# Kernel optimization log

Measured on AMD Instinct MI355X. Metric: run time of the kernel, lower is better.

The kernel has to match this reference:

```python
import jax, jax.numpy as jnp
import numpy as np

B, S, D, H = 2, 2048, 1024, 16
DK = D // H
DFF = 4 * D
EPS = 1e-6


def layer_norm(x, gamma, beta):
    mu = jnp.mean(x, axis=-1, keepdims=True)
    var = jnp.mean(jnp.square(x - mu), axis=-1, keepdims=True)
    return (x - mu) * jax.lax.rsqrt(var + EPS) * gamma + beta


def setup_inputs() -> dict:
    key = jax.random.key(0)
    ks = jax.random.split(key, 10)
    xavier = (6.0 / (D + D)) ** 0.5
    kaiming = (6.0 / D) ** 0.5
    kaiming2 = (6.0 / DFF) ** 0.5
    return {
        "batch_X": jax.random.normal(ks[0], (B, S, D), dtype=jnp.float32),
        "padding_mask": jax.random.randint(ks[1], (B, S), 0, 2, dtype=jnp.int32),
        "W_Q": jax.random.uniform(ks[2], (D, D), jnp.float32, -xavier, xavier),
        "W_K": jax.random.uniform(ks[3], (D, D), jnp.float32, -xavier, xavier),
        "W_V": jax.random.uniform(ks[4], (D, D), jnp.float32, -xavier, xavier),
        "W_O": jax.random.uniform(ks[5], (D, D), jnp.float32, -xavier, xavier),
        "W1": jax.random.uniform(ks[6], (D, DFF), jnp.float32, -kaiming, kaiming),
        "b1": jnp.zeros((DFF,), jnp.float32),
        "W2": jax.random.uniform(ks[7], (DFF, D), jnp.float32, -kaiming2, kaiming2),
        "b2": jnp.zeros((D,), jnp.float32),
        "gamma1": jnp.ones((D,), jnp.float32),
        "beta1": jnp.zeros((D,), jnp.float32),
        "gamma2": jnp.ones((D,), jnp.float32),
        "beta2": jnp.zeros((D,), jnp.float32),
    }


def reference(batch_X, padding_mask, W_Q, W_K, W_V, W_O, W1, b1, W2, b2,
              gamma1, beta1, gamma2, beta2):
    x = batch_X
    b, s, d = x.shape

    # --- multi-head self-attention (use_mask=False: padding mask only) ---
    q = (x @ W_Q).reshape(b, s, H, DK)
    k = (x @ W_K).reshape(b, s, H, DK)
    v = (x @ W_V).reshape(b, s, H, DK)
    scores = jnp.einsum("bqhd,bkhd->bhqk", q, k) / jnp.sqrt(jnp.float32(DK))
    # mask[b,i,j] = (padding_mask[b,i] == 0) for all j: whole query rows are
    # either fully masked (softmax -> NaN -> zeroed in the original) or
    # fully unmasked. Equivalent math: softmax then zero padded query rows.
    probs = jax.nn.softmax(scores, axis=-1)
    keep = (padding_mask != 0).astype(probs.dtype)[:, None, :, None]  # [B,1,S,1]
    probs = probs * keep
    ctx = jnp.einsum("bhqk,bkhd->bqhd", probs, v).reshape(b, s, d)
    attn_out = ctx @ W_O

    # --- residual + LN (dropout identity in eval) ---
    x = x + layer_norm(attn_out, gamma1, beta1)

    # --- FFN ---
    h = jax.nn.relu(x @ W1 + b1)
    ffn_out = h @ W2 + b2
    x = x + layer_norm(ffn_out, gamma2, beta2)
    return x
```

## Files before the change

kernel.cpp:

```cpp
#include <hip/hip_runtime.h>
#include <hip/hip_bf16.h>

#define B 2
#define S 2048
#define D 1024
#define H 16
#define DKh 64
#define DFF 4096
#define M (B*S)

typedef unsigned short u16;
typedef unsigned int u32;
typedef __attribute__((ext_vector_type(8))) short short8;
typedef __attribute__((ext_vector_type(4))) float f32x4;

__device__ __forceinline__ u16 f2bf(float f) {
  union { float f; unsigned u; } v; v.f = f;
  unsigned r = v.u + 0x7fffu + ((v.u >> 16) & 1u);
  return (u16)(r >> 16);
}

__device__ __forceinline__ float bf2f(u16 h) {
  union { u32 u; float f; } v; v.u = ((u32)h) << 16; return v.f;
}

__device__ __forceinline__ u32 pkbf2(float a, float b) {
  __hip_bfloat162 h = __float22bfloat162_rn(make_float2(a, b));
  return *reinterpret_cast<u32*>(&h);
}

__device__ __forceinline__ void gload16(const void* g, void* l) {
  __builtin_amdgcn_global_load_lds((const __attribute__((address_space(1))) void*)g,
                                   (__attribute__((address_space(3))) void*)l, 16, 0, 0);
}

#define SBAR()  __builtin_amdgcn_sched_barrier(0)
#define WBAR()  __builtin_amdgcn_s_barrier()

__device__ __forceinline__ void tcvt_body(const float* __restrict__ W,
    u16* __restrict__ Wt, int K, int N, int n0, int k0, u16 (*l)[65]) {
  const int tx = threadIdx.x & 63, ty = threadIdx.x >> 6;
#pragma unroll
  for (int j = 0; j < 16; ++j) {
    int r = j * 4 + ty;
    l[r][tx] = f2bf(W[(size_t)(k0 + r) * N + n0 + tx]);
  }
  __syncthreads();
#pragma unroll
  for (int j = 0; j < 16; ++j) {
    int r = j * 4 + ty;
    Wt[(size_t)(n0 + r) * K + k0 + tx] = l[tx][r];
  }
}

__global__ __launch_bounds__(256) void prep(const float* __restrict__ X,
    u16* __restrict__ Xb, const float* __restrict__ Wq, const float* __restrict__ Wk,
    const float* __restrict__ Wv, const float* __restrict__ Wo,
    u16* __restrict__ dQKV, u16* __restrict__ dO,
    const float* __restrict__ W1, u16* __restrict__ W1t,
    const float* __restrict__ W2, u16* __restrict__ W2t) {
  __shared__ u16 l[64][65];
  const int bid = blockIdx.x;
  if (bid < 4096) {
    int i = bid * 256 + threadIdx.x;
    float4 v = ((const float4*)X)[i];
    ushort4 o = make_ushort4(f2bf(v.x), f2bf(v.y), f2bf(v.z), f2bf(v.w));
    ((ushort4*)Xb)[i] = o;
  } else if (bid < 5120) {
    int bid2 = bid - 4096;
    int z = bid2 >> 8, r2 = bid2 & 255;
    const float* W = (z == 0) ? Wq : (z == 1) ? Wk : (z == 2) ? Wv : Wo;
    u16* Wt = (z < 3) ? dQKV + (size_t)z * D * D : dO;
    tcvt_body(W, Wt, D, D, (r2 & 15) * 64, (r2 >> 4) * 64, l);
  } else if (bid < 6144) {
    int r2 = bid - 5120;
    tcvt_body(W1, W1t, D, DFF, (r2 & 63) * 64, (r2 >> 6) * 64, l);
  } else {
    int r2 = bid - 6144;
    tcvt_body(W2, W2t, DFF, D, (r2 & 15) * 64, (r2 >> 4) * 64, l);
  }
}

__global__ __launch_bounds__(256) void vtrans(const u16* __restrict__ V,
                                              u16* __restrict__ Vt, int ld) {
  __shared__ u16 l[64][65];
  const int s0 = blockIdx.x * 64, by = blockIdx.y;
  const int b = by >> 4, h = by & 15;
  const int tx = threadIdx.x & 63, ty = threadIdx.x >> 6;
#pragma unroll
  for (int j = 0; j < 16; ++j) {
    int r = j * 4 + ty;
    l[r][tx] = V[(size_t)(b * S + s0 + r) * ld + h * DKh + tx];
  }
  __syncthreads();
#pragma unroll
  for (int j = 0; j < 16; ++j) {
    int r = j * 4 + ty;
    Vt[(size_t)(by * 64 + r) * S + s0 + tx] = l[tx][r];
  }
}

template<int EPI>
__global__ __launch_bounds__(512, 2) void gemm256(const u16* __restrict__ Ag,
    const u16* __restrict__ Bg, void* __restrict__ Cout,
    const float* __restrict__ bias, int Mm, int N, int ld, int Kper,
    int sCols, float qscl) {
  __shared__ u16 lA[2 * 16384];
  __shared__ u16 lB[2 * 16384];
  const int t = threadIdx.x;
  const int lane = t & 63, w = t >> 6;
  const int wm = w >> 2, wn = w & 3;
  const int g = lane >> 4, c = lane & 15;
  const int swz = (c & 7) << 4;

  const int gx = gridDim.x, gy = gridDim.y;
  const int orig = blockIdx.y * gx + blockIdx.x;
  const int qchunk = (gx * gy) >> 3;
  const int wg = (orig & 7) * qchunk + (orig >> 3);
  const int bn0 = (wg % gx) * 256, bm0 = (wg / gx) * 256;
  const int koff = blockIdx.z * Kper;
  const int nk = Kper >> 6;

  f32x4 acc[8][4] = {};
  short8 af[4][2], bf[2][2];

  auto stageA = [&](int h, int buf, int kt) {
#pragma unroll
    for (int i = 0; i < 2; ++i) {
      int chunk = i * 512 + t;
      int rh = chunk >> 3;
      int cb = (chunk & 7) * 16;
      int r = (rh & 63) + (h + 2 * (rh >> 6)) * 64;
      gload16(Ag + (size_t)(bm0 + r) * ld + koff + kt * 64 + ((cb ^ ((r & 7) << 4)) >> 1),
              (void*)((char*)lA + buf * 32768 + h * 16384 + chunk * 16));
    }
  };
  auto stageB = [&](int h, int buf, int kt) {
#pragma unroll
    for (int i = 0; i < 2; ++i) {
      int chunk = i * 512 + t;
      int rh = chunk >> 3;
      int cb = (chunk & 7) * 16;
      int r = (rh & 31) + (h + 2 * (rh >> 5)) * 32;
      gload16(Bg + (size_t)(bn0 + r) * ld + koff + kt * 64 + ((cb ^ ((r & 7) << 4)) >> 1),
              (void*)((char*)lB + buf * 32768 + h * 16384 + chunk * 16));
    }
  };

#define RDA(mh) { const char* lab = (const char*)lA + cur * 32768;                          \
  _Pragma("unroll") for (int mt2 = 0; mt2 < 4; ++mt2)                                       \
    _Pragma("unroll") for (int kc = 0; kc < 2; ++kc)                                        \
      af[mt2][kc] = *(const short8*)(lab + (wm * 64 + (mh) * 128 + mt2 * 16 + c) * 128      \
                                         + ((kc * 64 + g * 16) ^ swz)); }
#define RDB(nh) { const char* lbb = (const char*)lB + cur * 32768;                          \
  _Pragma("unroll") for (int nt2 = 0; nt2 < 2; ++nt2)                                       \
    _Pragma("unroll") for (int kc = 0; kc < 2; ++kc)                                        \
      bf[nt2][kc] = *(const short8*)(lbb + ((nh) * 128 + wn * 32 + nt2 * 16 + c) * 128      \
                                         + ((kc * 64 + g * 16) ^ swz)); }
#define QMFMA(mh, nh) { __builtin_amdgcn_s_setprio(1);                                      \
  _Pragma("unroll") for (int mt2 = 0; mt2 < 4; ++mt2)                                       \
    _Pragma("unroll") for (int nt2 = 0; nt2 < 2; ++nt2)                                     \
      _Pragma("unroll") for (int kc = 0; kc < 2; ++kc)                                      \
        acc[(mh) * 4 + mt2][(nh) * 2 + nt2] = __builtin_amdgcn_mfma_f32_16x16x32_bf16(      \
            af[mt2][kc], bf[nt2][kc], acc[(mh) * 4 + mt2][(nh) * 2 + nt2], 0, 0, 0);        \
  __builtin_amdgcn_s_setprio(0); }

  stageA(0, 0, 0); stageB(0, 0, 0); stageA(1, 0, 0); stageB(1, 0, 0);
  asm volatile("s_waitcnt vmcnt(4)" ::: "memory");
  SBAR(); WBAR(); SBAR();

  int cur = 0;
  for (int kt = 0; kt < nk; ++kt) {
    const bool more = (kt + 1 < nk);
    RDB(0); RDA(0);
    if (more) { stageA(0, cur ^ 1, kt + 1);
                asm volatile("s_waitcnt vmcnt(4)" ::: "memory"); }
    else      { asm volatile("s_waitcnt vmcnt(2)" ::: "memory"); }
    SBAR(); WBAR(); SBAR();
    QMFMA(0, 0);
    SBAR(); WBAR(); SBAR();
    RDA(1);
    if (more) { stageB(0, cur ^ 1, kt + 1);
                asm volatile("s_waitcnt vmcnt(4)" ::: "memory"); }
    else      { asm volatile("s_waitcnt vmcnt(0)" ::: "memory"); }
    SBAR(); WBAR(); SBAR();
    QMFMA(1, 0);
    SBAR(); WBAR(); SBAR();
    RDB(1);
    if (more) stageA(1, cur ^ 1, kt + 1);
    SBAR(); WBAR(); SBAR();
    QMFMA(1, 1);
    SBAR(); WBAR(); SBAR();
    RDA(0);
    if (more) { stageB(1, cur ^ 1, kt + 1);
                asm volatile("s_waitcnt vmcnt(4)" ::: "memory"); }
    SBAR(); WBAR(); SBAR();
    QMFMA(0, 1);
    SBAR(); WBAR(); SBAR();
    cur ^= 1;
  }
#undef RDA
#undef RDB
#undef QMFMA

  float* plane = (EPI == 1) ? ((float*)Cout + (size_t)blockIdx.z * Mm * N) : (float*)Cout;
#pragma unroll
  for (int mt = 0; mt < 8; ++mt) {
#pragma unroll
    for (int nt = 0; nt < 4; ++nt) {
      const int col = bn0 + wn * 64 + nt * 16 + c;
      float bv = (EPI == 2) ? bias[col] : 0.0f;
#pragma unroll
      for (int r = 0; r < 4; ++r) {
        const int row = bm0 + wm * 128 + mt * 16 + g * 4 + r;
        float v = acc[mt][nt][r];
        if (EPI == 2) v = fmaxf(v + bv, 0.0f);
        if (EPI == 0 && col < sCols) v *= qscl;
        if (EPI == 1) plane[(size_t)row * N + col] = v;
        else          ((u16*)Cout)[(size_t)row * N + col] = f2bf(v);
      }
    }
  }
}

__global__ __launch_bounds__(256) void attn_kernel(const u16* __restrict__ Q,
    const u16* __restrict__ Kp, const u16* __restrict__ Vt,
    const int* __restrict__ mask, u16* __restrict__ Ctx, int ldq) {
  __shared__ u16 lK[2][64 * 64];
  __shared__ u16 lV[2][64 * 64];
  __shared__ u16 lP[4 * 16 * 64];
  const int t = threadIdx.x, lane = t & 63, w = t >> 6;
  const int g = lane >> 4, c = lane & 15;
  const int gx = gridDim.x;
  const int orig = blockIdx.y * gx + blockIdx.x;
  const int qchunk = (gx * gridDim.y) >> 3;
  const int wg = (orig & 7) * qchunk + (orig >> 3);
  const int bx = wg % gx, by = wg / gx;
  const int b = by >> 4, h = by & 15;
  const int q0w = bx * 128 + w * 16;

  short8 qf[2][2];
#pragma unroll
  for (int s = 0; s < 2; ++s)
#pragma unroll
    for (int kc = 0; kc < 2; ++kc)
      qf[s][kc] = *(const short8*)&Q[(size_t)(b * S + q0w + s * 64 + c) * ldq + h * DKh + kc * 32 + g * 8];

  float lsum0 = 0.0f, lsum1 = 0.0f;
  f32x4 accO0[4] = {}, accO1[4] = {};

  auto stage = [&](int buf, int it) {
    const int kv0 = it * 64;
#pragma unroll
    for (int q = 0; q < 2; ++q) {
      int idx = q * 256 + t;
      int row = idx >> 3;
      int colb = (idx & 7) * 16;
      int scol = colb ^ ((row & 7) << 4);
      gload16(Kp + (size_t)(b * S + kv0 + row) * ldq + h * DKh + scol / 2,
              (void*)(&lK[buf][0] + idx * 8));
      gload16(Vt + (size_t)(by * 64 + row) * S + kv0 + scol / 2,
              (void*)(&lV[buf][0] + idx * 8));
    }
  };

  stage(0, 0);
  int cur = 0;
  for (int it = 0; it < S / 64; ++it) {
    __syncthreads();
    if (it + 1 < S / 64) stage(cur ^ 1, it + 1);

    f32x4 sc0[4], sc1[4];
#pragma unroll
    for (int ct = 0; ct < 4; ++ct) {
      int row = ct * 16 + c;
      short8 kf0 = *(const short8*)&lK[cur][row * 64 + (((0 * 64 + g * 16) ^ ((row & 7) << 4)) >> 1)];
      short8 kf1 = *(const short8*)&lK[cur][row * 64 + (((1 * 64 + g * 16) ^ ((row & 7) << 4)) >> 1)];
      f32x4 z0 = {0.f, 0.f, 0.f, 0.f};
      z0 = __builtin_amdgcn_mfma_f32_16x16x32_bf16(kf0, qf[0][0], z0, 0, 0, 0);
      z0 = __builtin_amdgcn_mfma_f32_16x16x32_bf16(kf1, qf[0][1], z0, 0, 0, 0);
      sc0[ct] = z0;
      f32x4 z1 = {0.f, 0.f, 0.f, 0.f};
      z1 = __builtin_amdgcn_mfma_f32_16x16x32_bf16(kf0, qf[1][0], z1, 0, 0, 0);
      z1 = __builtin_amdgcn_mfma_f32_16x16x32_bf16(kf1, qf[1][1], z1, 0, 0, 0);
      sc1[ct] = z1;
    }

    short8 pa0[2], pa1[2];
#pragma unroll
    for (int ct = 0; ct < 4; ++ct) {
      float p0 = __builtin_amdgcn_exp2f(sc0[ct][0]);
      float p1 = __builtin_amdgcn_exp2f(sc0[ct][1]);
      float p2 = __builtin_amdgcn_exp2f(sc0[ct][2]);
      float p3 = __builtin_amdgcn_exp2f(sc0[ct][3]);
      lsum0 += (p0 + p1) + (p2 + p3);
      uint2 pk;
      pk.x = pkbf2(p0, p1);
      pk.y = pkbf2(p2, p3);
      *(uint2*)&lP[w * 1024 + c * 64 + (((ct * 32 + g * 8) ^ ((c & 7) << 4)) >> 1)] = pk;
    }
#pragma unroll
    for (int kc = 0; kc < 2; ++kc)
      pa0[kc] = *(const short8*)&lP[w * 1024 + c * 64 + (((kc * 64 + g * 16) ^ ((c & 7) << 4)) >> 1)];
#pragma unroll
    for (int ct = 0; ct < 4; ++ct) {
      float p0 = __builtin_amdgcn_exp2f(sc1[ct][0]);
      float p1 = __builtin_amdgcn_exp2f(sc1[ct][1]);
      float p2 = __builtin_amdgcn_exp2f(sc1[ct][2]);
      float p3 = __builtin_amdgcn_exp2f(sc1[ct][3]);
      lsum1 += (p0 + p1) + (p2 + p3);
      uint2 pk;
      pk.x = pkbf2(p0, p1);
      pk.y = pkbf2(p2, p3);
      *(uint2*)&lP[w * 1024 + c * 64 + (((ct * 32 + g * 8) ^ ((c & 7) << 4)) >> 1)] = pk;
    }
#pragma unroll
    for (int kc = 0; kc < 2; ++kc)
      pa1[kc] = *(const short8*)&lP[w * 1024 + c * 64 + (((kc * 64 + g * 16) ^ ((c & 7) << 4)) >> 1)];

#pragma unroll
    for (int dt = 0; dt < 4; ++dt) {
#pragma unroll
      for (int kc = 0; kc < 2; ++kc) {
        int rowV = dt * 16 + c;
        int bcolV = (kc * 64 + g * 16) ^ ((rowV & 7) << 4);
        short8 vb = *(const short8*)&lV[cur][rowV * 64 + bcolV / 2];
        accO0[dt] = __builtin_amdgcn_mfma_f32_16x16x32_bf16(pa0[kc], vb, accO0[dt], 0, 0, 0);
        accO1[dt] = __builtin_amdgcn_mfma_f32_16x16x32_bf16(pa1[kc], vb, accO1[dt], 0, 0, 0);
      }
    }
    cur ^= 1;
  }

  lsum0 += __shfl_xor(lsum0, 16);
  lsum0 += __shfl_xor(lsum0, 32);
  lsum1 += __shfl_xor(lsum1, 16);
  lsum1 += __shfl_xor(lsum1, 32);

#pragma unroll
  for (int r = 0; r < 4; ++r) {
    int qrow = g * 4 + r;
    float lq0 = __shfl(lsum0, qrow);
    float lq1 = __shfl(lsum1, qrow);
    int q0 = q0w + qrow;
    int q1 = q0w + 64 + qrow;
    float inv0 = (mask[b * S + q0] != 0) ? (1.0f / lq0) : 0.0f;
    float inv1 = (mask[b * S + q1] != 0) ? (1.0f / lq1) : 0.0f;
#pragma unroll
    for (int dt = 0; dt < 4; ++dt) {
      Ctx[(size_t)(b * S + q0) * D + h * DKh + dt * 16 + c] = f2bf(accO0[dt][r] * inv0);
      Ctx[(size_t)(b * S + q1) * D + h * DKh + dt * 16 + c] = f2bf(accO1[dt][r] * inv1);
    }
  }
}

__global__ __launch_bounds__(256) void ln_res(const float* __restrict__ planes,
    int np, const float* __restrict__ bias, const float* __restrict__ XresF,
    const u16* __restrict__ XresB, const float* __restrict__ gamma,
    const float* __restrict__ beta, float* __restrict__ outF,
    u16* __restrict__ outB) {
  __shared__ float s1[4], s2[4];
  const int row = blockIdx.x, t = threadIdx.x;
  float4 y = ((const float4*)(planes + (size_t)row * D))[t];
  for (int j = 1; j < np; ++j) {
    const float4 y2 = ((const float4*)(planes + (size_t)j * M * D + (size_t)row * D))[t];
    y.x += y2.x; y.y += y2.y; y.z += y2.z; y.w += y2.w;
  }
  if (bias) {
    const float4 bb = ((const float4*)bias)[t];
    y.x += bb.x; y.y += bb.y; y.z += bb.z; y.w += bb.w;
  }
  float sm = y.x + y.y + y.z + y.w;
  float sq = y.x * y.x + y.y * y.y + y.z * y.z + y.w * y.w;
#pragma unroll
  for (int m2 = 1; m2 <= 32; m2 <<= 1) { sm += __shfl_xor(sm, m2); sq += __shfl_xor(sq, m2); }
  if ((t & 63) == 0) { s1[t >> 6] = sm; s2[t >> 6] = sq; }
  __syncthreads();
  float tot = s1[0] + s1[1] + s1[2] + s1[3];
  float tsq = s2[0] + s2[1] + s2[2] + s2[3];
  float mu = tot * (1.0f / D);
  float var = tsq * (1.0f / D) - mu * mu;
  float rstd = rsqrtf(var + 1e-6f);
  float4 xr;
  if (XresF) {
    xr = ((const float4*)(XresF + (size_t)row * D))[t];
  } else {
    ushort4 xb = ((const ushort4*)(XresB + (size_t)row * D))[t];
    xr.x = bf2f(xb.x); xr.y = bf2f(xb.y); xr.z = bf2f(xb.z); xr.w = bf2f(xb.w);
  }
  const float4 ga = ((const float4*)gamma)[t];
  const float4 be = ((const float4*)beta)[t];
  float4 o;
  o.x = xr.x + (y.x - mu) * rstd * ga.x + be.x;
  o.y = xr.y + (y.y - mu) * rstd * ga.y + be.y;
  o.z = xr.z + (y.z - mu) * rstd * ga.z + be.z;
  o.w = xr.w + (y.w - mu) * rstd * ga.w + be.w;
  if (outF) ((float4*)(outF + (size_t)row * D))[t] = o;
  if (outB) {
    ushort4 ob = make_ushort4(f2bf(o.x), f2bf(o.y), f2bf(o.z), f2bf(o.w));
    ((ushort4*)outB)[(size_t)row * (D / 4) + t] = ob;
  }
}

extern "C" void kernel_launch(void* const* d_in, const int* in_sizes, int n_in,
                              void* d_out, int out_size, void* d_ws, size_t ws_size,
                              hipStream_t stream) {
  const float* X   = (const float*)d_in[0];
  const int*   msk = (const int*)d_in[1];
  const float* WQ  = (const float*)d_in[2];
  const float* WK  = (const float*)d_in[3];
  const float* WV  = (const float*)d_in[4];
  const float* WO  = (const float*)d_in[5];
  const float* W1  = (const float*)d_in[6];
  const float* b1  = (const float*)d_in[7];
  const float* W2  = (const float*)d_in[8];
  const float* b2  = (const float*)d_in[9];
  const float* g1  = (const float*)d_in[10];
  const float* be1 = (const float*)d_in[11];
  const float* g2  = (const float*)d_in[12];
  const float* be2 = (const float*)d_in[13];
  float* out = (float*)d_out;
  const float SCL = 0.18033688011112042f;

  char* ws = (char*)d_ws;
  size_t off = 0;
  auto alloc = [&](size_t bytes) {
    void* p = ws + off;
    off += (bytes + 1023) & ~(size_t)1023;
    return p;
  };
  u16* Xb     = (u16*)alloc((size_t)M * D * 2);
  u16* WQKVt  = (u16*)alloc((size_t)3 * D * D * 2);
  u16* WOt    = (u16*)alloc((size_t)D * D * 2);
  u16* W1t    = (u16*)alloc((size_t)DFF * D * 2);
  u16* W2t    = (u16*)alloc((size_t)D * DFF * 2);
  u16* QKVb   = (u16*)alloc((size_t)M * 3 * D * 2);
  u16* Vt     = (u16*)alloc((size_t)B * H * DKh * S * 2);
  u16* Ctx    = (u16*)alloc((size_t)M * D * 2);
  u16* X1b    = (u16*)alloc((size_t)M * D * 2);
  u16* Hb     = (u16*)alloc((size_t)M * DFF * 2);
  float* PP   = (float*)QKVb;
  if (off > ws_size) return;
  size_t off4 = off;
  float* PP4 = (float*)(ws + off4);
  off4 += (size_t)4 * M * D * 4;
  const bool split4 = (off4 <= ws_size);

  dim3 blk(256), blk5(512);

  prep<<<dim3(7168), blk, 0, stream>>>(X, Xb, WQ, WK, WV, WO, WQKVt, WOt, W1, W1t, W2, W2t);
  gemm256<0><<<dim3(3 * D / 256, M / 256), blk5, 0, stream>>>(Xb, WQKVt, QKVb, nullptr, M, 3 * D, D, D, D, SCL);
  vtrans<<<dim3(S / 64, B * H), blk, 0, stream>>>(QKVb + 2 * D, Vt, 3 * D);
  attn_kernel<<<dim3(S / 128, B * H), blk, 0, stream>>>(QKVb, QKVb + D, Vt, msk, Ctx, 3 * D);
  gemm256<1><<<dim3(D / 256, M / 256, 2), blk5, 0, stream>>>(Ctx, WOt, PP, nullptr, M, D, D, D / 2, 0, 1.0f);
  ln_res<<<dim3(M), blk, 0, stream>>>(PP, 2, nullptr, X, nullptr, g1, be1, nullptr, X1b);
  gemm256<2><<<dim3(DFF / 256, M / 256), blk5, 0, stream>>>(X1b, W1t, Hb, b1, M, DFF, D, D, 0, 1.0f);
  if (split4) {
    gemm256<1><<<dim3(D / 256, M / 256, 4), blk5, 0, stream>>>(Hb, W2t, PP4, nullptr, M, D, DFF, DFF / 4, 0, 1.0f);
    ln_res<<<dim3(M), blk, 0, stream>>>(PP4, 4, b2, nullptr, X1b, g2, be2, out, nullptr);
  } else {
    gemm256<1><<<dim3(D / 256, M / 256, 2), blk5, 0, stream>>>(Hb, W2t, PP, nullptr, M, D, DFF, DFF / 2, 0, 1.0f);
    ln_res<<<dim3(M), blk, 0, stream>>>(PP, 2, b2, nullptr, X1b, g2, be2, out, nullptr);
  }
}
```

Before: 237.7 us.

## Split attention over KV sequence into two partitions with separate combine kernel

Attention now runs with a z-dimension of two, each block processing half of the key/value sequence and writing unnormalized fp32 partial outputs and row sums. A new combine kernel adds the partials, applies the mask and the normalization, and writes bf16 context. This doubles the number of attention blocks to fill the GPU better, but adds fp32 partial-output traffic and an extra kernel launch.

```diff
diff --git a/kernel.cpp b/kernel.cpp
--- a/kernel.cpp
+++ b/kernel.cpp
@@ -225,7 +225,7 @@
 
 __global__ __launch_bounds__(256) void attn_kernel(const u16* __restrict__ Q,
     const u16* __restrict__ Kp, const u16* __restrict__ Vt,
-    const int* __restrict__ mask, u16* __restrict__ Ctx, int ldq) {
+    float* __restrict__ OP, float* __restrict__ LS, int ldq) {
   __shared__ u16 lK[2][64 * 64];
   __shared__ u16 lV[2][64 * 64];
   __shared__ u16 lP[4 * 16 * 64];
@@ -237,6 +237,7 @@
   const int wg = (orig & 7) * qchunk + (orig >> 3);
   const int bx = wg % gx, by = wg / gx;
   const int b = by >> 4, h = by & 15;
+  const int z = blockIdx.z;
   const int q0w = bx * 128 + w * 16;
 
   short8 qf[2][2];
@@ -250,7 +251,7 @@
   f32x4 accO0[4] = {}, accO1[4] = {};
 
   auto stage = [&](int buf, int it) {
-    const int kv0 = it * 64;
+    const int kv0 = (z * (S / 128) + it) * 64;
 #pragma unroll
     for (int q = 0; q < 2; ++q) {
       int idx = q * 256 + t;
@@ -266,9 +267,10 @@
 
   stage(0, 0);
   int cur = 0;
-  for (int it = 0; it < S / 64; ++it) {
+  const int NIT = S / 128;
+  for (int it = 0; it < NIT; ++it) {
     __syncthreads();
-    if (it + 1 < S / 64) stage(cur ^ 1, it + 1);
+    if (it + 1 < NIT) stage(cur ^ 1, it + 1);
 
     f32x4 sc0[4], sc1[4];
 #pragma unroll
@@ -337,21 +339,36 @@
   lsum1 += __shfl_xor(lsum1, 16);
   lsum1 += __shfl_xor(lsum1, 32);
 
+  const size_t zO = (size_t)z * M * D;
 #pragma unroll
   for (int r = 0; r < 4; ++r) {
     int qrow = g * 4 + r;
-    float lq0 = __shfl(lsum0, qrow);
-    float lq1 = __shfl(lsum1, qrow);
-    int q0 = q0w + qrow;
-    int q1 = q0w + 64 + qrow;
-    float inv0 = (mask[b * S + q0] != 0) ? (1.0f / lq0) : 0.0f;
-    float inv1 = (mask[b * S + q1] != 0) ? (1.0f / lq1) : 0.0f;
+    const size_t base0 = (size_t)(b * S + q0w + qrow) * D + h * DKh;
+    const size_t base1 = (size_t)(b * S + q0w + 64 + qrow) * D + h * DKh;
 #pragma unroll
     for (int dt = 0; dt < 4; ++dt) {
-      Ctx[(size_t)(b * S + q0) * D + h * DKh + dt * 16 + c] = f2bf(accO0[dt][r] * inv0);
-      Ctx[(size_t)(b * S + q1) * D + h * DKh + dt * 16 + c] = f2bf(accO1[dt][r] * inv1);
-    }
-  }
+      OP[zO + base0 + dt * 16 + c] = accO0[dt][r];
+      OP[zO + base1 + dt * 16 + c] = accO1[dt][r];
+    }
+  }
+  if (lane < 16) {
+    LS[(size_t)z * M * H + (size_t)(b * S + q0w + lane) * H + h] = lsum0;
+    LS[(size_t)z * M * H + (size_t)(b * S + q0w + 64 + lane) * H + h] = lsum1;
+  }
+}
+
+__global__ __launch_bounds__(256) void attn_combine(const float* __restrict__ OP,
+    const float* __restrict__ LS, const int* __restrict__ mask,
+    u16* __restrict__ Ctx) {
+  const int row = blockIdx.x, t = threadIdx.x;
+  const int h = t >> 4;
+  float l = LS[(size_t)row * H + h] + LS[(size_t)M * H + (size_t)row * H + h];
+  float inv = (mask[row] != 0) ? (1.0f / l) : 0.0f;
+  const float4 a = ((const float4*)(OP + (size_t)row * D))[t];
+  const float4 bb = ((const float4*)(OP + (size_t)M * D + (size_t)row * D))[t];
+  ushort4 o = make_ushort4(f2bf((a.x + bb.x) * inv), f2bf((a.y + bb.y) * inv),
+                           f2bf((a.z + bb.z) * inv), f2bf((a.w + bb.w) * inv));
+  ((ushort4*)(Ctx + (size_t)row * D))[t] = o;
 }
 
 __global__ __launch_bounds__(256) void ln_res(const float* __restrict__ planes,
@@ -439,6 +456,8 @@
   u16* Ctx    = (u16*)alloc((size_t)M * D * 2);
   u16* X1b    = (u16*)alloc((size_t)M * D * 2);
   u16* Hb     = (u16*)alloc((size_t)M * DFF * 2);
+  float* LS   = (float*)alloc((size_t)2 * M * H * 4);
+  float* OP   = (float*)Hb;
   float* PP   = (float*)QKVb;
   if (off > ws_size) return;
   size_t off4 = off;
@@ -451,7 +470,8 @@
   prep<<<dim3(7168), blk, 0, stream>>>(X, Xb, WQ, WK, WV, WO, WQKVt, WOt, W1, W1t, W2, W2t);
   gemm256<0><<<dim3(3 * D / 256, M / 256), blk5, 0, stream>>>(Xb, WQKVt, QKVb, nullptr, M, 3 * D, D, D, D, SCL);
   vtrans<<<dim3(S / 64, B * H), blk, 0, stream>>>(QKVb + 2 * D, Vt, 3 * D);
-  attn_kernel<<<dim3(S / 128, B * H), blk, 0, stream>>>(QKVb, QKVb + D, Vt, msk, Ctx, 3 * D);
+  attn_kernel<<<dim3(S / 128, B * H, 2), blk, 0, stream>>>(QKVb, QKVb + D, Vt, OP, LS, 3 * D);
+  attn_combine<<<dim3(M), blk, 0, stream>>>(OP, LS, msk, Ctx);
   gemm256<1><<<dim3(D / 256, M / 256, 2), blk5, 0, stream>>>(Ctx, WOt, PP, nullptr, M, D, D, D / 2, 0, 1.0f);
   ln_res<<<dim3(M), blk, 0, stream>>>(PP, 2, nullptr, X, nullptr, g1, be1, nullptr, X1b);
   gemm256<2><<<dim3(DFF / 256, M / 256), blk5, 0, stream>>>(X1b, W1t, Hb, b1, M, DFF, D, D, 0, 1.0f);
```

After: 248.6 us. 1.05x slower.
